# Kernel tuning notes

Measured on AMD Instinct MI355X. Metric: run time of the kernel, lower is better.

Reference implementation:

```python
import jax, jax.numpy as jnp
import numpy as np

HEADS = 6
WSIZE = 8
SHIFTS = 4
EPS = 1e-5


def conv1x1(x, w, b=None):
    # x: (B,C,H,W), w: (O,C)
    y = jnp.einsum('bchw,oc->bohw', x, w)
    if b is not None:
        y = y + b[None, :, None, None]
    return y


def spatial_shift(x):
    # ShiftConv2d1 depthwise fixed-kernel conv == per-group spatial shift with zero pad
    C = x.shape[1]
    g = C // 5
    x0, x1, x2, x3, x4 = (x[:, :g], x[:, g:2 * g], x[:, 2 * g:3 * g],
                          x[:, 3 * g:4 * g], x[:, 4 * g:])
    left = jnp.pad(x0[:, :, :, 1:], ((0, 0), (0, 0), (0, 0), (0, 1)))   # kernel (1,2)
    right = jnp.pad(x1[:, :, :, :-1], ((0, 0), (0, 0), (0, 0), (1, 0)))  # kernel (1,0)
    up = jnp.pad(x2[:, :, 1:, :], ((0, 0), (0, 0), (0, 1), (0, 0)))      # kernel (2,1)
    down = jnp.pad(x3[:, :, :-1, :], ((0, 0), (0, 0), (1, 0), (0, 0)))   # kernel (0,1)
    return jnp.concatenate([left, right, up, down, x4], axis=1)


def window_attn(xb, ws, heads, shifts):
    # xb: (B, 2*heads*c, H, W); self-similarity attention q@q^T (no separate K, no scaling)
    if shifts > 0:
        xb = jnp.roll(xb, (-(ws // 2), -(ws // 2)), axis=(2, 3))
    b, c2, H, W = xb.shape
    cd = c2 // (2 * heads)
    nh, nw = H // ws, W // ws
    t = xb.reshape(b, 2, heads, cd, nh, ws, nw, ws)
    t = t.transpose(1, 0, 4, 6, 2, 5, 7, 3).reshape(2, b * nh * nw, heads, ws * ws, cd)
    q, v = t[0], t[1]
    atn = jax.nn.softmax(jnp.einsum('whnc,whmc->whnm', q, q), axis=-1)
    o = jnp.einsum('whnm,whmc->whnc', atn, v)
    o = o.reshape(b, nh, nw, heads, ws, ws, cd)
    o = o.transpose(0, 3, 6, 1, 4, 2, 5).reshape(b, heads * cd, H, W)
    if shifts > 0:
        o = jnp.roll(o, (ws // 2, ws // 2), axis=(2, 3))
    return o


def setup_inputs() -> dict:
    key = jax.random.key(0)
    ks = jax.random.split(key, 8)
    B, C, H, W = 2, 180, 256, 256
    s = 0.05
    return {
        'x': jax.random.normal(ks[0], (B, C, H, W), jnp.float32),
        'w0': jax.random.normal(ks[1], (2 * C, C), jnp.float32) * s,
        'b0': jnp.zeros((2 * C,), jnp.float32),
        'w1': jax.random.normal(ks[2], (C, 2 * C), jnp.float32) * s,
        'b1': jnp.zeros((C,), jnp.float32),
        'w_in': jax.random.normal(ks[3], (2 * C, C), jnp.float32) * s,
        'b_in': jnp.zeros((2 * C,), jnp.float32),
        'bn_g': jnp.ones((2 * C,), jnp.float32),
        'bn_b': jnp.zeros((2 * C,), jnp.float32),
        'w_out': jax.random.normal(ks[4], (C, C), jnp.float32) * s,
        'b_out': jnp.zeros((C,), jnp.float32),
    }


def reference(x, w0, b0, w1, b1, w_in, b_in, bn_g, bn_b, w_out, b_out):
    # --- LFE (shift-conv FFN), exp_ratio=2, relu ---
    y = conv1x1(spatial_shift(x), w0, b0)
    y = jax.nn.relu(y)
    y = conv1x1(spatial_shift(y), w1, b1)
    x = y + x
    # --- GMSA (3 parallel shifted-window self-similarity attentions) ---
    z = conv1x1(x, w_in, b_in)
    mu = z.mean(axis=(0, 2, 3), keepdims=True)
    var = z.var(axis=(0, 2, 3), keepdims=True)  # biased, matching BN training forward
    z = (z - mu) / jnp.sqrt(var + EPS) * bn_g[None, :, None, None] + bn_b[None, :, None, None]
    cs = z.shape[1] // 3
    sizes = [WSIZE // 4, WSIZE // 2, WSIZE]
    outs = [window_attn(z[:, i * cs:(i + 1) * cs], sizes[i], HEADS, SHIFTS)
            for i in range(3)]
    out = conv1x1(jnp.concatenate(outs, axis=1), w_out, b_out)
    return out + x
```

## Files before the change

### kernel.cpp

```cpp
#include <hip/hip_runtime.h>
#include <hip/hip_bf16.h>

#define HWSZ 65536
#define NPIX 131072

typedef unsigned short u16;
typedef __bf16 bf16x8 __attribute__((ext_vector_type(8)));
typedef float f32x4 __attribute__((ext_vector_type(4)));
typedef unsigned short u16x2 __attribute__((ext_vector_type(2)));
typedef unsigned short u16x4 __attribute__((ext_vector_type(4)));
typedef unsigned short u16x8 __attribute__((ext_vector_type(8)));
typedef unsigned short u16x8u __attribute__((ext_vector_type(8), aligned(4)));

__device__ inline u16 f2bf(float f) {
    unsigned int x = __builtin_bit_cast(unsigned int, f);
    unsigned int r = x + 0x7FFFu + ((x >> 16) & 1u);
    return (u16)(r >> 16);
}
__device__ inline float bf2f(u16 u) {
    unsigned int x = ((unsigned int)u) << 16;
    return __builtin_bit_cast(float, x);
}

__global__ __launch_bounds__(256) void prep_w(
    const float* __restrict__ w0, const float* __restrict__ w1,
    const float* __restrict__ wi, const float* __restrict__ wo,
    u16* __restrict__ W0p, u16* __restrict__ W1p,
    u16* __restrict__ Wip, u16* __restrict__ Wop)
{
    const int i = blockIdx.x * 256 + threadIdx.x;
    {
        const int r = i / 192, c = i % 192;
        const bool ok = (r < 360) && (c < 180);
        W0p[i] = ok ? f2bf(w0[r * 180 + c]) : (u16)0;
        Wip[i] = ok ? f2bf(wi[r * 180 + c]) : (u16)0;
    }
    {
        const int r = i / 384, c = i % 384;
        W1p[i] = (r < 180 && c < 360) ? f2bf(w1[r * 360 + c]) : (u16)0;
    }
    if (i < 36864) {
        const int r = i / 192, c = i % 192;
        Wop[i] = (r < 180 && c < 180) ? f2bf(wo[r * 180 + c]) : (u16)0;
    }
}

template<int CI, int CO, int G, int INM, int XSTR, bool RELU, int RES, int OUTM, int OSTR, bool COSPLIT>
__global__ __launch_bounds__(256, 4) void conv_v9(
    const void* __restrict__ Xv, const u16* __restrict__ Wp,
    const float* __restrict__ bias, const void* __restrict__ Rv,
    void* __restrict__ Yv)
{
    constexpr int CI_PAD = ((CI + 31) / 32) * 32;
    constexpr int NSTEP  = CI_PAD / 32;
    constexpr int LDK    = 40;

    __shared__ u16 Xt[2][64 * LDK];

    const int tid = threadIdx.x;
    const int bid = blockIdx.x;
    int px_tile, co0;
    if (COSPLIT) {
        co0     = ((bid >> 3) & 1) * 192;
        px_tile = ((bid >> 4) << 3) | (bid & 7);
    } else {
        co0 = 0; px_tile = bid;
    }
    const int p0   = px_tile << 6;
    const int b    = p0 >> 16;
    const int pix0 = p0 & 65535;
    const int h    = pix0 >> 8;
    const int w0c  = pix0 & 255;
    const int lane = tid & 63, wid = tid >> 6;
    const int lr = lane & 15, lg = lane >> 4;
    const int co_wave = co0 + wid * 48;

    const float* Xf = (const float*)Xv + (size_t)b * CI * HWSZ;
    const u16*   Xh = (const u16*)Xv;

    const int xn  = tid & 63;
    const int k4a = tid >> 6;

    auto loadX = [&](int kt, u16x4 (&r)[2]) {
        #pragma unroll
        for (int it = 0; it < 2; ++it) {
            const int k4 = k4a + it * 4;
            const int c0 = kt + k4 * 4;
            u16x4 v = {0, 0, 0, 0};
            if (c0 < CI) {
                int dh = 0, dw = 0;
                if (G > 0) {
                    const int g = c0 / G;
                    if      (g == 0) dw = 1;
                    else if (g == 1) dw = -1;
                    else if (g == 2) dh = 1;
                    else if (g == 3) dh = -1;
                }
                const int hh = h + dh;
                const int wp = w0c + xn + dw;
                if (hh >= 0 && hh < 256 && wp >= 0 && wp < 256) {
                    if constexpr (INM == 1) {
                        v = *(const u16x4*)&Xh[(size_t)((b << 16) | (hh << 8) | wp) * XSTR + c0];
                    } else {
                        const float* xs = Xf + (size_t)c0 * HWSZ + hh * 256 + wp;
                        #pragma unroll
                        for (int j = 0; j < 4; ++j) v[j] = f2bf(xs[(size_t)j * HWSZ]);
                    }
                }
            }
            r[it] = v;
        }
    };

    auto loadW = [&](int kt, bf16x8 (&a)[3]) {
        #pragma unroll
        for (int mf = 0; mf < 3; ++mf)
            a[mf] = *(const bf16x8*)&Wp[(size_t)(co_wave + mf * 16 + lr) * CI_PAD + kt + lg * 8];
    };

    auto writeLDS = [&](u16x4 (&r)[2], int buf) {
        *(u16x4*)&Xt[buf][xn * LDK + k4a * 4]       = r[0];
        *(u16x4*)&Xt[buf][xn * LDK + (k4a + 4) * 4] = r[1];
    };

    f32x4 acc[3][4] = {};
    u16x4 raw[2][2];
    bf16x8 af[2][3];

    loadX(0, raw[0]);
    loadW(0, af[0]);
    writeLDS(raw[0], 0);

    #pragma unroll
    for (int s = 0; s < NSTEP; ++s) {
        const int cur = s & 1, nxt = cur ^ 1;
        __syncthreads();
        if (s + 1 < NSTEP) {
            loadX((s + 1) * 32, raw[nxt]);
            loadW((s + 1) * 32, af[nxt]);
        }
        bf16x8 bfr[4];
        #pragma unroll
        for (int nf = 0; nf < 4; ++nf)
            bfr[nf] = *(const bf16x8*)&Xt[cur][(nf * 16 + lr) * LDK + lg * 8];
        #pragma unroll
        for (int mf = 0; mf < 3; ++mf)
            #pragma unroll
            for (int nf = 0; nf < 4; ++nf)
                acc[mf][nf] = __builtin_amdgcn_mfma_f32_16x16x32_bf16(
                    af[cur][mf], bfr[nf], acc[mf][nf], 0, 0, 0);
        if (s + 1 < NSTEP) writeLDS(raw[nxt], nxt);
    }

    const float* Rf = (const float*)Rv;
    const u16*   Rh = (const u16*)Rv;
    #pragma unroll
    for (int mf = 0; mf < 3; ++mf) {
        const int co_b = co_wave + mf * 16 + lg * 4;
        if (co_b >= CO) continue;
        #pragma unroll
        for (int nf = 0; nf < 4; ++nf) {
            const int pl = pix0 + nf * 16 + lr;
            const size_t pg = (size_t)p0 + nf * 16 + lr;
            float v[4];
            #pragma unroll
            for (int r = 0; r < 4; ++r) {
                v[r] = acc[mf][nf][r] + bias[co_b + r];
                if (RELU) v[r] = fmaxf(v[r], 0.f);
            }
            if (RES == 1) {
                #pragma unroll
                for (int r = 0; r < 4; ++r)
                    v[r] += Rf[((size_t)(b * CO + co_b + r)) * HWSZ + pl];
            }
            if (RES == 2) {
                u16x4 rr = *(const u16x4*)&Rh[pg * 180 + co_b];
                #pragma unroll
                for (int r = 0; r < 4; ++r) v[r] += bf2f(rr[r]);
            }
            if (OUTM == 1) {
                u16x4 o;
                #pragma unroll
                for (int r = 0; r < 4; ++r) o[r] = f2bf(v[r]);
                *(u16x4*)&((u16*)Yv)[pg * OSTR + co_b] = o;
            } else {
                #pragma unroll
                for (int r = 0; r < 4; ++r)
                    ((float*)Yv)[((size_t)(b * CO + co_b + r)) * HWSZ + pl] = v[r];
            }
        }
    }
}

template<int CI, int CO, int G, int XSTR, bool RELU, int RES, int OUTM, int OSTR, bool COSPLIT>
__global__ __launch_bounds__(256) void conv_v12(
    const u16* __restrict__ Xh, const u16* __restrict__ Wp,
    const float* __restrict__ bias, const void* __restrict__ Rv,
    void* __restrict__ Yv)
{
    constexpr int CI_PAD = ((CI + 31) / 32) * 32;
    constexpr int NSTEP  = CI_PAD / 32;

    const int tid = threadIdx.x;
    const int bid = blockIdx.x;
    int px_tile, co0;
    if (COSPLIT) {
        co0     = ((bid >> 3) & 1) * 192;
        px_tile = ((bid >> 4) << 3) | (bid & 7);
    } else {
        co0 = 0; px_tile = bid;
    }
    const int p0   = px_tile << 6;
    const int b    = p0 >> 16;
    const int pix0 = p0 & 65535;
    const int lane = tid & 63, wid = tid >> 6;
    const int lr = lane & 15, lg = lane >> 4;
    const int co_wave = co0 + wid * 48;

    int hhv[4], wpv[4];
    long pbase[4];
    #pragma unroll
    for (int nf = 0; nf < 4; ++nf) {
        const int pix = pix0 + nf * 16 + lr;
        hhv[nf] = pix >> 8; wpv[nf] = pix & 255;
        pbase[nf] = (long)((b << 16) | pix) * XSTR;
    }

    auto shiftOf = [&](int g, int nf, int& off, bool& ok) {
        off = 0; ok = true;
        if      (g == 0) { off =  XSTR;        ok = (wpv[nf] < 255); }
        else if (g == 1) { off = -XSTR;        ok = (wpv[nf] > 0);   }
        else if (g == 2) { off =  (XSTR << 8); ok = (hhv[nf] < 255); }
        else if (g == 3) { off = -(XSTR << 8); ok = (hhv[nf] > 0);   }
    };
    auto loadv = [&](long idx) -> u16x8 {
        return __builtin_bit_cast(u16x8, *(const u16x8u*)&Xh[idx]);
    };

    auto loadFrags = [&](int s, bf16x8 (&bfr)[4], bf16x8 (&af)[3]) {
        const int c0 = s * 32 + lg * 8;
        #pragma unroll
        for (int nf = 0; nf < 4; ++nf) {
            u16x8 a = {0, 0, 0, 0, 0, 0, 0, 0};
            if constexpr (G > 0) {
                const int g0 = (c0 < CI) ? (c0 / G) : 4;
                int off0; bool ok0;
                shiftOf(g0, nf, off0, ok0);
                if (ok0) a = loadv(pbase[nf] + off0 + c0);
                const int ce = (c0 + 7 < CI) ? (c0 + 7) : (CI - 1);
                const int g1 = (c0 < CI) ? (ce / G) : 4;
                if (g1 != g0) {
                    int off1; bool ok1;
                    shiftOf(g1, nf, off1, ok1);
                    u16x8 b2 = {0, 0, 0, 0, 0, 0, 0, 0};
                    if (ok1) b2 = loadv(pbase[nf] + off1 + c0);
                    const int Bb = g1 * G;
                    #pragma unroll
                    for (int j = 0; j < 8; ++j)
                        if (c0 + j >= Bb) a[j] = b2[j];
                }
            } else {
                a = loadv(pbase[nf] + c0);
            }
            bfr[nf] = __builtin_bit_cast(bf16x8, a);
        }
        #pragma unroll
        for (int mf = 0; mf < 3; ++mf)
            af[mf] = *(const bf16x8*)&Wp[(size_t)(co_wave + mf * 16 + lr) * CI_PAD + c0];
    };

    f32x4 acc[3][4] = {};
    bf16x8 bfr[2][4], af[2][3];

    loadFrags(0, bfr[0], af[0]);

    #pragma unroll
    for (int s = 0; s < NSTEP; ++s) {
        const int cur = s & 1, nxt = cur ^ 1;
        if (s + 1 < NSTEP) loadFrags(s + 1, bfr[nxt], af[nxt]);
        #pragma unroll
        for (int mf = 0; mf < 3; ++mf)
            #pragma unroll
            for (int nf = 0; nf < 4; ++nf)
                acc[mf][nf] = __builtin_amdgcn_mfma_f32_16x16x32_bf16(
                    af[cur][mf], bfr[cur][nf], acc[mf][nf], 0, 0, 0);
    }

    const float* Rf = (const float*)Rv;
    const u16*   Rh = (const u16*)Rv;
    #pragma unroll
    for (int mf = 0; mf < 3; ++mf) {
        const int co_b = co_wave + mf * 16 + lg * 4;
        if (co_b >= CO) continue;
        #pragma unroll
        for (int nf = 0; nf < 4; ++nf) {
            const int pl = pix0 + nf * 16 + lr;
            const size_t pg = (size_t)p0 + nf * 16 + lr;
            float v[4];
            #pragma unroll
            for (int r = 0; r < 4; ++r) {
                v[r] = acc[mf][nf][r] + bias[co_b + r];
                if (RELU) v[r] = fmaxf(v[r], 0.f);
            }
            if (RES == 1) {
                #pragma unroll
                for (int r = 0; r < 4; ++r)
                    v[r] += Rf[((size_t)(b * CO + co_b + r)) * HWSZ + pl];
            }
            if (RES == 2) {
                u16x4 rr = *(const u16x4*)&Rh[pg * 180 + co_b];
                #pragma unroll
                for (int r = 0; r < 4; ++r) v[r] += bf2f(rr[r]);
            }
            if (OUTM == 1) {
                u16x4 o;
                #pragma unroll
                for (int r = 0; r < 4; ++r) o[r] = f2bf(v[r]);
                *(u16x4*)&((u16*)Yv)[pg * OSTR + co_b] = o;
            } else {
                #pragma unroll
                for (int r = 0; r < 4; ++r)
                    ((float*)Yv)[((size_t)(b * CO + co_b + r)) * HWSZ + pl] = v[r];
            }
        }
    }
}

__global__ __launch_bounds__(256) void bn_part(const u16* __restrict__ zt,
                                               float* __restrict__ part)
{
    const int tid = threadIdx.x;
    const int oc  = tid & 63;
    const int pp  = tid >> 6;
    if (oc >= 45) return;
    const int stripe = blockIdx.x * 4 + pp;
    const int pb = blockIdx.x * 1024 + pp;
    float s[8] = {}, q[8] = {};
    for (int i = 0; i < 256; ++i) {
        const int p = pb + i * 4;
        u16x8 t = *(const u16x8*)&zt[(size_t)p * 360 + oc * 8];
        #pragma unroll
        for (int j = 0; j < 8; ++j) {
            float v = bf2f(t[j]);
            s[j] += v; q[j] += v * v;
        }
    }
    float* pr = part + ((size_t)stripe * 45 + oc) * 16;
    #pragma unroll
    for (int j = 0; j < 8; ++j) { pr[j] = s[j]; pr[8 + j] = q[j]; }
}

__global__ __launch_bounds__(256) void bn_fin(const float* __restrict__ part,
                                              const float* __restrict__ g,
                                              const float* __restrict__ bb,
                                              float* __restrict__ sc,
                                              float* __restrict__ sh)
{
    const int oc = blockIdx.x;
    const int t  = threadIdx.x;
    const float* p1 = part + ((size_t)t * 45 + oc) * 16;
    const float* p2 = part + ((size_t)(t + 256) * 45 + oc) * 16;
    float v[16];
    #pragma unroll
    for (int k = 0; k < 16; ++k) v[k] = p1[k] + p2[k];
    #pragma unroll
    for (int k = 0; k < 16; ++k)
        for (int m = 32; m; m >>= 1) v[k] += __shfl_xor(v[k], m, 64);
    __shared__ float red[4][16];
    if ((t & 63) == 0) {
        #pragma unroll
        for (int k = 0; k < 16; ++k) red[t >> 6][k] = v[k];
    }
    __syncthreads();
    if (t == 0) {
        const float invN = 1.f / (float)NPIX;
        #pragma unroll
        for (int j = 0; j < 8; ++j) {
            const int c = oc * 8 + j;
            float su = red[0][j] + red[1][j] + red[2][j] + red[3][j];
            float sq = red[0][8+j] + red[1][8+j] + red[2][8+j] + red[3][8+j];
            float mean = su * invN;
            float var  = sq * invN - mean * mean;
            float istd = 1.f / sqrtf(var + 1e-5f);
            float s = g[c] * istd;
            sc[c] = s;
            sh[c] = bb[c] - mean * s;
        }
    }
}

template<int WS>
__global__ __launch_bounds__(256) void attn_v2(
    const u16* __restrict__ zt, const float* __restrict__ scale,
    const float* __restrict__ shiftc, u16* __restrict__ ot, int chunk)
{
    constexpr int NP  = WS * WS;
    constexpr int GPB = 256 / NP;
    constexpr int SH  = WS / 2;
    constexpr int NW  = 256 / WS;

    __shared__ float qs[256 * 12];
    __shared__ float vs[256 * 12];

    const int tid = threadIdx.x;
    const int lg  = tid / NP;
    const int n   = tid % NP;
    const int gidx = blockIdx.x * GPB + lg;

    const int head = gidx % 6;
    const int win  = gidx / 6;
    const int wcol = win % NW;
    const int tmp  = win / NW;
    const int wrow = tmp % NW;
    const int b    = tmp / NW;

    const int i = n / WS, j = n % WS;
    const int hh = (wrow * WS + i + SH) & 255;
    const int ww = (wcol * WS + j + SH) & 255;
    const size_t zrow = (size_t)((b << 16) | (hh << 8) | ww) * 360;

    const int cq = chunk * 120 + head * 10;
    const int cv = cq + 60;

    float q[10];
    float* qrow = &qs[tid * 12];
    float* vrow = &vs[tid * 12];
    #pragma unroll
    for (int c2 = 0; c2 < 5; ++c2) {
        u16x2 uq = *(const u16x2*)&zt[zrow + cq + c2 * 2];
        u16x2 uv = *(const u16x2*)&zt[zrow + cv + c2 * 2];
        float q0 = bf2f(uq[0]) * scale[cq + c2 * 2]     + shiftc[cq + c2 * 2];
        float q1 = bf2f(uq[1]) * scale[cq + c2 * 2 + 1] + shiftc[cq + c2 * 2 + 1];
        float v0 = bf2f(uv[0]) * scale[cv + c2 * 2]     + shiftc[cv + c2 * 2];
        float v1 = bf2f(uv[1]) * scale[cv + c2 * 2 + 1] + shiftc[cv + c2 * 2 + 1];
        q[c2 * 2] = q0; q[c2 * 2 + 1] = q1;
        qrow[c2 * 2] = q0; qrow[c2 * 2 + 1] = q1;
        vrow[c2 * 2] = v0; vrow[c2 * 2 + 1] = v1;
    }
    qrow[10] = 0.f; qrow[11] = 0.f;
    vrow[10] = 0.f; vrow[11] = 0.f;
    __syncthreads();

    const float* qg = &qs[(lg * NP) * 12];
    const float* vg = &vs[(lg * NP) * 12];

    float mx = -1e30f;
    for (int m = 0; m < NP; ++m) {
        f32x4 a0 = *(const f32x4*)&qg[m * 12];
        f32x4 a1 = *(const f32x4*)&qg[m * 12 + 4];
        f32x4 a2 = *(const f32x4*)&qg[m * 12 + 8];
        float d = q[0]*a0[0] + q[1]*a0[1] + q[2]*a0[2] + q[3]*a0[3]
                + q[4]*a1[0] + q[5]*a1[1] + q[6]*a1[2] + q[7]*a1[3]
                + q[8]*a2[0] + q[9]*a2[1];
        mx = fmaxf(mx, d);
    }
    float s = 0.f;
    float o[10] = {};
    for (int m = 0; m < NP; ++m) {
        f32x4 a0 = *(const f32x4*)&qg[m * 12];
        f32x4 a1 = *(const f32x4*)&qg[m * 12 + 4];
        f32x4 a2 = *(const f32x4*)&qg[m * 12 + 8];
        float d = q[0]*a0[0] + q[1]*a0[1] + q[2]*a0[2] + q[3]*a0[3]
                + q[4]*a1[0] + q[5]*a1[1] + q[6]*a1[2] + q[7]*a1[3]
                + q[8]*a2[0] + q[9]*a2[1];
        float e = __expf(d - mx);
        s += e;
        f32x4 b0 = *(const f32x4*)&vg[m * 12];
        f32x4 b1 = *(const f32x4*)&vg[m * 12 + 4];
        f32x4 b2 = *(const f32x4*)&vg[m * 12 + 8];
        o[0] += e * b0[0]; o[1] += e * b0[1]; o[2] += e * b0[2]; o[3] += e * b0[3];
        o[4] += e * b1[0]; o[5] += e * b1[1]; o[6] += e * b1[2]; o[7] += e * b1[3];
        o[8] += e * b2[0]; o[9] += e * b2[1];
    }
    const float inv = 1.f / s;
    u16* orow = ot + (size_t)((b << 16) | (hh << 8) | ww) * 180 + chunk * 60 + head * 10;
    #pragma unroll
    for (int c2 = 0; c2 < 5; ++c2) {
        u16x2 ov;
        ov[0] = f2bf(o[c2 * 2] * inv);
        ov[1] = f2bf(o[c2 * 2 + 1] * inv);
        *(u16x2*)&orow[c2 * 2] = ov;
    }
}

extern "C" void kernel_launch(void* const* d_in, const int* in_sizes, int n_in,
                              void* d_out, int out_size, void* d_ws, size_t ws_size,
                              hipStream_t stream)
{
    const float* x     = (const float*)d_in[0];
    const float* w0    = (const float*)d_in[1];
    const float* b0    = (const float*)d_in[2];
    const float* w1    = (const float*)d_in[3];
    const float* b1    = (const float*)d_in[4];
    const float* w_in  = (const float*)d_in[5];
    const float* b_in  = (const float*)d_in[6];
    const float* bn_g  = (const float*)d_in[7];
    const float* bn_b  = (const float*)d_in[8];
    const float* w_out = (const float*)d_in[9];
    const float* b_out = (const float*)d_in[10];
    float* out = (float*)d_out;

    u16* y   = (u16*)d_ws;
    u16* x1b = y   + (size_t)NPIX * 360;
    u16* ot  = x1b + (size_t)NPIX * 180;
    u16* W0p = ot  + (size_t)NPIX * 180;
    u16* Wip = W0p + 384 * 192;
    u16* W1p = Wip + 384 * 192;
    u16* Wop = W1p + 192 * 384;
    float* part   = (float*)(Wop + 192 * 192);
    float* scale  = part + 512 * 45 * 16;
    float* shiftc = scale + 360;
    u16* zt = y;

    dim3 blk(256);

    prep_w<<<dim3(288), blk, 0, stream>>>(w0, w1, w_in, w_out, W0p, W1p, Wip, Wop);

    conv_v9<180, 360, 36, 0, 0,   true,  0, 1, 360, true>
        <<<dim3(4096), blk, 0, stream>>>(x, W0p, b0, nullptr, y);
    conv_v12<360, 180, 72, 360, false, 1, 1, 180, false>
        <<<dim3(2048), blk, 0, stream>>>(y, W1p, b1, x, x1b);
    conv_v12<180, 360, 0,  180, false, 0, 1, 360, true>
        <<<dim3(4096), blk, 0, stream>>>(x1b, Wip, b_in, nullptr, zt);
    bn_part<<<dim3(128), blk, 0, stream>>>(zt, part);
    bn_fin<<<dim3(45), blk, 0, stream>>>(part, bn_g, bn_b, scale, shiftc);
    attn_v2<2><<<dim3(3072), blk, 0, stream>>>(zt, scale, shiftc, ot, 0);
    attn_v2<4><<<dim3(3072), blk, 0, stream>>>(zt, scale, shiftc, ot, 1);
    attn_v2<8><<<dim3(3072), blk, 0, stream>>>(zt, scale, shiftc, ot, 2);
    conv_v12<180, 180, 0,  180, false, 2, 0, 0, false>
        <<<dim3(2048), blk, 0, stream>>>(ot, Wop, b_out, x1b, out);
}
```

Before: 427.4 us.

## Fuse second FFN conv and input projection conv into one kernel

Adds a kernel, conv23, that computes the shifted 360->180 conv with bias and residual, then keeps the 64-pixel x1 tile in shared memory and runs the 180->360 input projection on it directly. This removes one kernel launch and the round trip of reading x1b back from global memory. zt now gets its own workspace buffer because it can no longer alias y, which the fused kernel is still reading. The fused kernel loads the shifted inputs directly from global memory without LDS staging, holds more accumulator registers, and has an extra barrier, so occupancy and load efficiency may drop compared with the separate kernels.

After: 449.9 us. 5.3% more time.

```diff
diff --git a/kernel.cpp b/kernel.cpp
--- a/kernel.cpp
+++ b/kernel.cpp
@@ -192,6 +192,135 @@
     }
 }
 
+__global__ __launch_bounds__(256) void conv23(
+    const u16* __restrict__ Yh, const u16* __restrict__ W1p,
+    const float* __restrict__ b1, const float* __restrict__ xres,
+    const u16* __restrict__ Wip, const float* __restrict__ b_in,
+    u16* __restrict__ x1b, u16* __restrict__ zt)
+{
+    constexpr int LDR = 204;
+    __shared__ u16 X1[64 * LDR];
+
+    const int tid = threadIdx.x;
+    const int p0   = blockIdx.x << 6;
+    const int b    = p0 >> 16;
+    const int pix0 = p0 & 65535;
+    const int lane = tid & 63, wid = tid >> 6;
+    const int lr = lane & 15, lg = lane >> 4;
+    const int co_wave = wid * 48;
+
+    for (int e = tid; e < 64 * 12; e += 256) {
+        const int px = e / 12, c = 180 + (e % 12);
+        X1[px * LDR + c] = 0;
+    }
+
+    int hhv[4], wpv[4];
+    long pbase[4];
+    #pragma unroll
+    for (int nf = 0; nf < 4; ++nf) {
+        const int pix = pix0 + nf * 16 + lr;
+        hhv[nf] = pix >> 8; wpv[nf] = pix & 255;
+        pbase[nf] = (long)((b << 16) | pix) * 360;
+    }
+
+    auto shiftOf = [&](int g, int nf, int& off, bool& ok) {
+        off = 0; ok = true;
+        if      (g == 0) { off =  360;        ok = (wpv[nf] < 255); }
+        else if (g == 1) { off = -360;        ok = (wpv[nf] > 0);   }
+        else if (g == 2) { off =  (360 << 8); ok = (hhv[nf] < 255); }
+        else if (g == 3) { off = -(360 << 8); ok = (hhv[nf] > 0);   }
+    };
+    auto loadv = [&](long idx) -> u16x8 {
+        return __builtin_bit_cast(u16x8, *(const u16x8u*)&Yh[idx]);
+    };
+
+    f32x4 acc[3][4] = {};
+    #pragma unroll
+    for (int s = 0; s < 12; ++s) {
+        const int c0 = s * 32 + lg * 8;
+        bf16x8 bfr[4];
+        #pragma unroll
+        for (int nf = 0; nf < 4; ++nf) {
+            u16x8 a = {0, 0, 0, 0, 0, 0, 0, 0};
+            const int g0 = (c0 < 360) ? (c0 / 72) : 4;
+            int off0; bool ok0;
+            shiftOf(g0, nf, off0, ok0);
+            if (c0 < 360 && ok0) a = loadv(pbase[nf] + off0 + c0);
+            bfr[nf] = __builtin_bit_cast(bf16x8, a);
+        }
+        bf16x8 af[3];
+        #pragma unroll
+        for (int mf = 0; mf < 3; ++mf)
+            af[mf] = *(const bf16x8*)&W1p[(size_t)(co_wave + mf * 16 + lr) * 384 + c0];
+        #pragma unroll
+        for (int mf = 0; mf < 3; ++mf)
+            #pragma unroll
+            for (int nf = 0; nf < 4; ++nf)
+                acc[mf][nf] = __builtin_amdgcn_mfma_f32_16x16x32_bf16(
+                    af[mf], bfr[nf], acc[mf][nf], 0, 0, 0);
+    }
+
+    #pragma unroll
+    for (int mf = 0; mf < 3; ++mf) {
+        const int co_b = co_wave + mf * 16 + lg * 4;
+        if (co_b >= 180) continue;
+        #pragma unroll
+        for (int nf = 0; nf < 4; ++nf) {
+            const int pl = pix0 + nf * 16 + lr;
+            const size_t pg = (size_t)p0 + nf * 16 + lr;
+            const int px = nf * 16 + lr;
+            u16x4 o;
+            #pragma unroll
+            for (int r = 0; r < 4; ++r) {
+                float v = acc[mf][nf][r] + b1[co_b + r]
+                        + xres[((size_t)(b * 180 + co_b + r)) * HWSZ + pl];
+                o[r] = f2bf(v);
+            }
+            *(u16x4*)&x1b[pg * 180 + co_b] = o;
+            *(u16x4*)&X1[px * LDR + co_b]  = o;
+        }
+    }
+    __syncthreads();
+
+    #pragma unroll
+    for (int coh = 0; coh < 2; ++coh) {
+        const int co2 = (wid + coh * 4) * 48;
+        f32x4 acc2[3][4] = {};
+        #pragma unroll
+        for (int s = 0; s < 6; ++s) {
+            const int c0 = s * 32 + lg * 8;
+            bf16x8 bfr[4];
+            #pragma unroll
+            for (int nf = 0; nf < 4; ++nf)
+                bfr[nf] = *(const bf16x8*)&X1[(nf * 16 + lr) * LDR + c0];
+            bf16x8 af[3];
+            #pragma unroll
+            for (int mf = 0; mf < 3; ++mf)
+                af[mf] = *(const bf16x8*)&Wip[(size_t)(co2 + mf * 16 + lr) * 192 + c0];
+            #pragma unroll
+            for (int mf = 0; mf < 3; ++mf)
+                #pragma unroll
+                for (int nf = 0; nf < 4; ++nf)
+                    acc2[mf][nf] = __builtin_amdgcn_mfma_f32_16x16x32_bf16(
+                        af[mf], bfr[nf], acc2[mf][nf], 0, 0, 0);
+        }
+        #pragma unroll
+        for (int mf = 0; mf < 3; ++mf) {
+            const int co_b = co2 + mf * 16 + lg * 4;
+            if (co_b >= 360) continue;
+            #pragma unroll
+            for (int nf = 0; nf < 4; ++nf) {
+                const size_t pg = (size_t)p0 + nf * 16 + lr;
+                u16x4 o;
+                #pragma unroll
+                for (int r = 0; r < 4; ++r)
+                    o[r] = f2bf(acc2[mf][nf][r] + b_in[co_b + r]);
+                *(u16x4*)&zt[pg * 360 + co_b] = o;
+            }
+        }
+    }
+}
+
 template<int CI, int CO, int G, int XSTR, bool RELU, int RES, int OUTM, int OSTR, bool COSPLIT>
 __global__ __launch_bounds__(256) void conv_v12(
     const u16* __restrict__ Xh, const u16* __restrict__ Wp,
@@ -501,7 +630,8 @@
     float* out = (float*)d_out;
 
     u16* y   = (u16*)d_ws;
-    u16* x1b = y   + (size_t)NPIX * 360;
+    u16* zt  = y   + (size_t)NPIX * 360;
+    u16* x1b = zt  + (size_t)NPIX * 360;
     u16* ot  = x1b + (size_t)NPIX * 180;
     u16* W0p = ot  + (size_t)NPIX * 180;
     u16* Wip = W0p + 384 * 192;
@@ -510,7 +640,6 @@
     float* part   = (float*)(Wop + 192 * 192);
     float* scale  = part + 512 * 45 * 16;
     float* shiftc = scale + 360;
-    u16* zt = y;
 
     dim3 blk(256);
 
@@ -518,10 +647,7 @@
 
     conv_v9<180, 360, 36, 0, 0,   true,  0, 1, 360, true>
         <<<dim3(4096), blk, 0, stream>>>(x, W0p, b0, nullptr, y);
-    conv_v12<360, 180, 72, 360, false, 1, 1, 180, false>
-        <<<dim3(2048), blk, 0, stream>>>(y, W1p, b1, x, x1b);
-    conv_v12<180, 360, 0,  180, false, 0, 1, 360, true>
-        <<<dim3(4096), blk, 0, stream>>>(x1b, Wip, b_in, nullptr, zt);
+    conv23<<<dim3(2048), blk, 0, stream>>>(y, W1p, b1, x, Wip, b_in, x1b, zt);
     bn_part<<<dim3(128), blk, 0, stream>>>(zt, part);
     bn_fin<<<dim3(45), blk, 0, stream>>>(part, bn_g, bn_b, scale, shiftc);
     attn_v2<2><<<dim3(3072), blk, 0, stream>>>(zt, scale, shiftc, ot, 0);
```
